# Optimization experiments

Hardware: AMD Instinct MI355X
Metric: run time of the kernel (lower is better)

## Reference

```python
import jax, jax.numpy as jnp
import numpy as np

B, S, D, H, AD, E = 4, 2048, 1024, 2048, 128, 8

def _ln(x, g, b, eps=1e-5):
    m = jnp.mean(x, axis=-1, keepdims=True)
    v = jnp.var(x, axis=-1, keepdims=True)
    return (x - m) * jax.lax.rsqrt(v + eps) * g + b

def setup_inputs() -> dict:
    key = jax.random.key(0)
    ks = jax.random.split(key, 12)
    scale = 1.0 / D ** 0.5
    ascale = scale * 0.01
    ead = 0.01 / AD ** 0.5
    return {
        'x': jax.random.normal(ks[0], (B, S, D), jnp.float32),
        'expert_weights': jax.random.uniform(ks[1], (B, S, E), jnp.float32),
        'Wu': jax.random.normal(ks[2], (H, D), jnp.float32) * scale,
        'bu': jnp.zeros((H,), jnp.float32),
        'Wg': jax.random.normal(ks[3], (H, D), jnp.float32) * scale,
        'bg': jnp.zeros((H,), jnp.float32),
        'Wd': jax.random.normal(ks[4], (D, H), jnp.float32) * scale,
        'bd': jnp.zeros((D,), jnp.float32),
        'Wpre': jax.random.normal(ks[5], (AD, D), jnp.float32) * ascale,
        'bpre': jnp.zeros((AD,), jnp.float32),
        'Wpost': jax.random.normal(ks[6], (AD, H), jnp.float32) * ascale,
        'bpost': jnp.zeros((AD,), jnp.float32),
        'ln_g': jnp.ones((AD,), jnp.float32),
        'ln_b': jnp.zeros((AD,), jnp.float32),
        'Wap': jax.random.normal(ks[7], (H, AD), jnp.float32) * ascale,
        'A': jax.random.normal(ks[8], (E, AD, AD), jnp.float32) * ead,
        'eg': jnp.ones((E, AD), jnp.float32),
        'eb': jnp.zeros((E, AD), jnp.float32),
        'Wp': jax.random.normal(ks[9], (H, AD), jnp.float32) * ead,
        'Wo': jax.random.normal(ks[10], (D, H), jnp.float32) * ead,
    }

def reference(x, expert_weights, Wu, bu, Wg, bg, Wd, bd, Wpre, bpre, Wpost, bpost, ln_g, ln_b, Wap, A, eg, eb, Wp, Wo):
    # ---- SharedExpertMLP ----
    up = x @ Wu.T + bu                      # [B,S,H]
    gate = x @ Wg.T + bg
    hidden = jax.nn.silu(gate) * up
    adapt_in = _ln(x @ Wpre.T + bpre, ln_g, ln_b)        # [B,S,AD]
    adapt_out = _ln(hidden @ Wpost.T + bpost, ln_g, ln_b)
    aw = jnp.einsum('bsa,bta->bst', adapt_in, adapt_out)  # [B,S,S]
    aw = jax.nn.silu(jnp.clip(aw, -5.0, 5.0))
    adapt = jnp.einsum('bst,bta->bsa', aw, adapt_in)
    hidden = hidden + 0.1 * (adapt @ Wap.T)
    shared = hidden @ Wd.T + bd                           # [B,S,D]
    # ---- expert branch (vectorized over experts) ----
    pre = x @ Wpre.T + bpre                               # [B,S,AD] (no adapt_norm here, as in torch)
    h = jnp.einsum('bsa,eca->ebsc', pre, A)               # per-expert adapter linear
    h = _ln(h, eg[:, None, None, :], eb[:, None, None, :])
    wmask = jnp.where(expert_weights > 0, expert_weights, 0.0)  # [B,S,E]
    hw = jnp.einsum('ebsa,bse->bsa', h, wmask)            # weighted combine before shared projections
    Wc = Wo @ Wp                                          # [D,AD]: output_proj(expert_proj(.))
    contrib = hw @ Wc.T                                   # [B,S,D]
    # sum_i w_i * (shared + 0.1*mask_i*expert_i) = shared*sum(w) + 0.1*sum(w_i*expert_i)
    return shared * jnp.sum(expert_weights, axis=-1, keepdims=True) + 0.1 * contrib
```

## Files before the change

kernel.cpp:

```cpp
#include <hip/hip_runtime.h>
#include <math.h>

#define BB 4
#define SS 2048
#define DD 1024
#define HH 2048
#define AD 128
#define EE 8
#define MM (BB*SS)
#define PS 136

typedef unsigned short u16;
typedef short bf16x8 __attribute__((ext_vector_type(8)));
typedef float f32x4 __attribute__((ext_vector_type(4)));
typedef float f32x16 __attribute__((ext_vector_type(16)));

__device__ __forceinline__ float silu_f(float x){ return x / (1.f + __expf(-x)); }

__device__ __forceinline__ u16 f2bf(float f){
    union { float f; unsigned u; } c; c.f = f;
    unsigned r = (c.u + 0x7FFFu + ((c.u >> 16) & 1u)) >> 16;
    return (u16)r;
}

__device__ __forceinline__ void gld16(const u16* g, u16* l){
    __builtin_amdgcn_global_load_lds((const __attribute__((address_space(1))) void*)g,
                                     (__attribute__((address_space(3))) void*)l, 16, 0, 0);
}

#define VMCNT(n) asm volatile("s_waitcnt vmcnt(" #n ")" ::: "memory")

__global__ __launch_bounds__(256,2) void mfma_sk(
    const u16* __restrict__ A, const u16* __restrict__ B, float* __restrict__ P,
    int M, int K, int S, long sA, long sB, long sC, long sSplit)
{
    __shared__ __align__(16) u16 As[128*32];
    __shared__ __align__(16) u16 Bs[128*32];
    const int t = threadIdx.x;
    const int lane = t & 63;
    const int wv = t >> 6;
    const int s = blockIdx.x;
    const int m0 = blockIdx.y * 128;
    const u16* Ab = A + (long)blockIdx.z * sA;
    const u16* Bb = B + (long)blockIdx.z * sB;
    const int srow = t >> 2, scol = (t & 3) * 8;
    const int Ks = K / S, kBeg = s * Ks;
    const u16* ga0 = Ab + (long)(m0 + srow) * K + scol + kBeg;
    const u16* ga1 = ga0 + 64L * K;
    const u16* gb0 = Bb + (long)srow * K + scol + kBeg;
    const u16* gb1 = gb0 + 64L * K;
    u16* la0 = As + t * 8;  u16* la1 = As + 2048 + t * 8;
    u16* lb0 = Bs + t * 8;  u16* lb1 = Bs + 2048 + t * 8;
    const int fr = lane & 15, q = lane >> 4;
    const int wm = (wv & 1) * 64, wn = (wv >> 1) * 64;

    f32x4 acc[4][4] = {};
    for (int k0 = 0; k0 < Ks; k0 += 32) {
        gld16(ga0 + k0, la0);
        gld16(ga1 + k0, la1);
        gld16(gb0 + k0, lb0);
        gld16(gb1 + k0, lb1);
        __syncthreads();
        bf16x8 af[4], bfr[4];
        #pragma unroll
        for (int i = 0; i < 4; ++i) af[i]  = *(const bf16x8*)&As[(wm + i*16 + fr)*32 + q*8];
        #pragma unroll
        for (int i = 0; i < 4; ++i) bfr[i] = *(const bf16x8*)&Bs[(wn + i*16 + fr)*32 + q*8];
        #pragma unroll
        for (int mi = 0; mi < 4; ++mi)
            #pragma unroll
            for (int ni = 0; ni < 4; ++ni)
                acc[mi][ni] = __builtin_amdgcn_mfma_f32_16x16x32_bf16(af[mi], bfr[ni], acc[mi][ni], 0, 0, 0);
        __syncthreads();
    }

    float* Pf = P + (long)s * sSplit + (long)blockIdx.z * sC;
    #pragma unroll
    for (int mi = 0; mi < 4; ++mi)
        #pragma unroll
        for (int ni = 0; ni < 4; ++ni) {
            const int col = wn + ni*16 + fr;
            #pragma unroll
            for (int r = 0; r < 4; ++r) {
                const int row = m0 + wm + mi*16 + q*4 + r;
                Pf[(long)row * 128 + col] = acc[mi][ni][r];
            }
        }
}

__global__ __launch_bounds__(512,2) void mfma_upgate(
    const u16* __restrict__ X, const u16* __restrict__ Wu_, const u16* __restrict__ Wg_,
    const float* __restrict__ bu, const float* __restrict__ bg, u16* __restrict__ H)
{
    __shared__ __align__(16) u16 lds[65536];
    const int t = threadIdx.x, lane = t & 63, wv = t >> 6;
    const int l31 = lane & 31, kh = lane >> 5;
    const int wr = wv >> 2, wc = wv & 3;
    const int m0 = blockIdx.y * 256, n0 = blockIdx.x * 128;

    const int srow = t >> 2;
    const int gcol = (((t & 3) ^ ((t >> 3) & 3)) * 8);
    const u16* gx0 = X   + (long)(m0 + srow) * DD + gcol;
    const u16* gx1 = gx0 + 128L * DD;
    const u16* gu  = Wu_ + (long)(n0 + srow) * DD + gcol;
    const u16* gg  = Wg_ + (long)(n0 + srow) * DD + gcol;
    const int st8 = t * 8;

    const int sw3 = (l31 >> 1) & 3;
    int offA[4][2], offB[2];
    #pragma unroll
    for (int m = 0; m < 4; ++m)
        #pragma unroll
        for (int ks = 0; ks < 2; ++ks)
            offA[m][ks] = (wr*128 + m*32 + l31)*32 + (((ks*2 + kh) ^ sw3) * 8);
    #pragma unroll
    for (int ks = 0; ks < 2; ++ks)
        offB[ks] = (wc*32 + l31)*32 + (((ks*2 + kh) ^ sw3) * 8);

    f32x16 accU[4] = {};
    f32x16 accG[4] = {};

    auto stage = [&](int tb) {
        u16* Lb = lds + (tb & 3) * 16384;
        const int k0 = tb * 32;
        gld16(gx0 + k0, Lb + st8);
        gld16(gx1 + k0, Lb + 4096 + st8);
        gld16(gu  + k0, Lb + 8192 + st8);
        gld16(gg  + k0, Lb + 12288 + st8);
    };

    auto compute = [&](int tb) {
        const u16* Lb = lds + (tb & 3) * 16384;
        bf16x8 a[4][2], uf[2], gf[2];
        #pragma unroll
        for (int ks = 0; ks < 2; ++ks) {
            uf[ks] = *(const bf16x8*)&Lb[8192  + offB[ks]];
            gf[ks] = *(const bf16x8*)&Lb[12288 + offB[ks]];
        }
        #pragma unroll
        for (int m = 0; m < 4; ++m)
            #pragma unroll
            for (int ks = 0; ks < 2; ++ks)
                a[m][ks] = *(const bf16x8*)&Lb[offA[m][ks]];
        __builtin_amdgcn_s_setprio(1);
        #pragma unroll
        for (int m = 0; m < 4; ++m)
            #pragma unroll
            for (int ks = 0; ks < 2; ++ks) {
                accU[m] = __builtin_amdgcn_mfma_f32_32x32x16_bf16(a[m][ks], uf[ks], accU[m], 0, 0, 0);
                accG[m] = __builtin_amdgcn_mfma_f32_32x32x16_bf16(a[m][ks], gf[ks], accG[m], 0, 0, 0);
            }
        __builtin_amdgcn_s_setprio(0);
    };

    stage(0); stage(1); stage(2);

    #pragma unroll 1
    for (int tt = 0; tt < 29; ++tt) {
        VMCNT(8);
        __builtin_amdgcn_s_barrier();
        __builtin_amdgcn_sched_barrier(0);
        stage(tt + 3);
        compute(tt);
    }
    VMCNT(8);
    __builtin_amdgcn_s_barrier();
    __builtin_amdgcn_sched_barrier(0);
    compute(29);
    VMCNT(4);
    __builtin_amdgcn_s_barrier();
    __builtin_amdgcn_sched_barrier(0);
    compute(30);
    VMCNT(0);
    __builtin_amdgcn_s_barrier();
    __builtin_amdgcn_sched_barrier(0);
    compute(31);

    const int col = n0 + wc*32 + l31;
    const float bub = bu[col], bgb = bg[col];
    u16* Hp = H + (long)(m0 + wr*128) * HH + col;
    #pragma unroll
    for (int m = 0; m < 4; ++m)
        #pragma unroll
        for (int r = 0; r < 16; ++r) {
            const int rowl = m*32 + (r & 3) + 8*(r >> 2) + 4*kh;
            const float u = accU[m][r] + bub;
            const float g = accG[m][r] + bgb;
            Hp[(long)rowl * HH] = f2bf(silu_f(g) * u);
        }
}

__global__ __launch_bounds__(256,2) void mfma_final(
    const u16* __restrict__ Hh, const u16* __restrict__ Wd_,
    const u16* __restrict__ Ac, const u16* __restrict__ Wcat,
    const float* __restrict__ bd, const float* __restrict__ sumw,
    float* __restrict__ out)
{
    __shared__ __align__(16) u16 lds[24576];
    const int t = threadIdx.x, lane = t & 63, wv = t >> 6;
    const int l31 = lane & 31, kh = lane >> 5;
    const int wr = wv & 1, wc = wv >> 1;
    const int m0 = blockIdx.y * 128, n0 = blockIdx.x * 128;

    const int srow = t >> 2;
    const int gcol = (((t & 3) ^ ((t >> 3) & 3)) * 8);
    const u16* gA1 = Hh   + (long)(m0 + srow) * HH  + gcol;
    const u16* gB1 = Wd_  + (long)(n0 + srow) * HH  + gcol;
    const u16* gA2 = Ac   + (long)(m0 + srow) * 256 + gcol;
    const u16* gB2 = Wcat + (long)(n0 + srow) * 256 + gcol;
    const int st8 = t * 8;

    const int sw3 = (l31 >> 1) & 3;
    int offA[2][2], offB[2][2];
    #pragma unroll
    for (int m = 0; m < 2; ++m)
        #pragma unroll
        for (int ks = 0; ks < 2; ++ks) {
            const int ko = ((ks*2 + kh) ^ sw3) * 8;
            offA[m][ks] =        (wr*64 + m*32 + l31)*32 + ko;
            offB[m][ks] = 4096 + (wc*64 + m*32 + l31)*32 + ko;
        }

    f32x16 acc[2][2]  = {};
    f32x16 acc2[2][2] = {};

    auto stage = [&](int tk) {
        u16* Lb = lds + (tk % 3) * 8192;
        if (tk < 64) {
            const int k0 = tk * 32;
            gld16(gA1 + k0,           Lb + st8);
            gld16(gA1 + 64L*HH + k0,  Lb + 2048 + st8);
            gld16(gB1 + k0,           Lb + 4096 + st8);
            gld16(gB1 + 64L*HH + k0,  Lb + 6144 + st8);
        } else {
            const int k0 = (tk - 64) * 32;
            gld16(gA2 + k0,           Lb + st8);
            gld16(gA2 + 64L*256 + k0, Lb + 2048 + st8);
            gld16(gB2 + k0,           Lb + 4096 + st8);
            gld16(gB2 + 64L*256 + k0, Lb + 6144 + st8);
        }
    };

    auto compute = [&](int tk, f32x16 (&A)[2][2]) {
        const u16* Lb = lds + (tk % 3) * 8192;
        bf16x8 a[2][2], b[2][2];
        #pragma unroll
        for (int m = 0; m < 2; ++m)
            #pragma unroll
            for (int ks = 0; ks < 2; ++ks) {
                a[m][ks] = *(const bf16x8*)&Lb[offA[m][ks]];
                b[m][ks] = *(const bf16x8*)&Lb[offB[m][ks]];
            }
        __builtin_amdgcn_s_setprio(1);
        #pragma unroll
        for (int m = 0; m < 2; ++m)
            #pragma unroll
            for (int n = 0; n < 2; ++n)
                #pragma unroll
                for (int ks = 0; ks < 2; ++ks)
                    A[m][n] = __builtin_amdgcn_mfma_f32_32x32x16_bf16(a[m][ks], b[n][ks], A[m][n], 0, 0, 0);
        __builtin_amdgcn_s_setprio(0);
    };

    stage(0); stage(1);
    #pragma unroll 1
    for (int tt = 0; tt < 70; ++tt) {
        VMCNT(4);
        __builtin_amdgcn_s_barrier();
        __builtin_amdgcn_sched_barrier(0);
        stage(tt + 2);
        if (tt < 64) compute(tt, acc); else compute(tt, acc2);
    }
    VMCNT(4);
    __builtin_amdgcn_s_barrier();
    __builtin_amdgcn_sched_barrier(0);
    compute(70, acc2);
    VMCNT(0);
    __builtin_amdgcn_s_barrier();
    __builtin_amdgcn_sched_barrier(0);
    compute(71, acc2);

    #pragma unroll
    for (int n = 0; n < 2; ++n) {
        const int col = n0 + wc*64 + n*32 + l31;
        const float bdc = bd[col];
        #pragma unroll
        for (int m = 0; m < 2; ++m)
            #pragma unroll
            for (int r = 0; r < 16; ++r) {
                const int row = m0 + wr*64 + m*32 + (r & 3) + 8*(r >> 2) + 4*kh;
                out[(long)row * DD + col] =
                    sumw[row] * (acc[m][n][r] + bdc) + 0.1f * acc2[m][n][r];
            }
    }
}

__global__ __launch_bounds__(256,2) void flash_pv(
    const u16* __restrict__ ai, const u16* __restrict__ ao,
    const u16* __restrict__ aiT, float* __restrict__ adaptP)
{
    __shared__ __align__(16) u16 As[128*32];
    __shared__ __align__(16) u16 Bs[128*32];
    __shared__ __align__(16) u16 Psh[128*PS];
    const int t = threadIdx.x, lane = t & 63, wv = t >> 6;
    const int fr = lane & 15, q = lane >> 4;
    const int wm = (wv & 1) * 64, wn = (wv >> 1) * 64;
    const int tg = blockIdx.x, s0 = blockIdx.y * 128, b = blockIdx.z;
    const u16* aib  = ai  + (long)b * SS * AD;
    const u16* aob  = ao  + (long)b * SS * AD;
    const u16* aiTb = aiT + (long)b * AD * SS;
    const int srow = t >> 2, scol = (t & 3) * 8;
    u16* la0 = As + t * 8;  u16* la1 = As + 2048 + t * 8;
    u16* lb0 = Bs + t * 8;  u16* lb1 = Bs + 2048 + t * 8;
    const u16* ga0 = aib + (long)(s0 + srow) * AD + scol;
    const u16* ga1 = ga0 + 64L * AD;

    f32x4 vacc[4][4] = {};
    for (int ti = 0; ti < 2; ++ti) {
        const int t0 = tg * 256 + ti * 128;
        const u16* gb0 = aob + (long)(t0 + srow) * AD + scol;
        const u16* gb1 = gb0 + 64L * AD;
        f32x4 acc[4][4] = {};
        for (int k0 = 0; k0 < AD; k0 += 32) {
            gld16(ga0 + k0, la0);
            gld16(ga1 + k0, la1);
            gld16(gb0 + k0, lb0);
            gld16(gb1 + k0, lb1);
            __syncthreads();
            bf16x8 af[4], bfr[4];
            #pragma unroll
            for (int i = 0; i < 4; ++i) af[i]  = *(const bf16x8*)&As[(wm + i*16 + fr)*32 + q*8];
            #pragma unroll
            for (int i = 0; i < 4; ++i) bfr[i] = *(const bf16x8*)&Bs[(wn + i*16 + fr)*32 + q*8];
            #pragma unroll
            for (int mi = 0; mi < 4; ++mi)
                #pragma unroll
                for (int ni = 0; ni < 4; ++ni)
                    acc[mi][ni] = __builtin_amdgcn_mfma_f32_16x16x32_bf16(af[mi], bfr[ni], acc[mi][ni], 0, 0, 0);
            __syncthreads();
        }
        #pragma unroll
        for (int mi = 0; mi < 4; ++mi)
            #pragma unroll
            for (int ni = 0; ni < 4; ++ni)
                #pragma unroll
                for (int r = 0; r < 4; ++r) {
                    float v = acc[mi][ni][r];
                    v = fminf(fmaxf(v, -5.f), 5.f);
                    Psh[(wm + mi*16 + q*4 + r)*PS + wn + ni*16 + fr] = f2bf(silu_f(v));
                }
        __syncthreads();
        #pragma unroll
        for (int kk = 0; kk < 4; ++kk) {
            bf16x8 pf[4], bi[4];
            #pragma unroll
            for (int mi = 0; mi < 4; ++mi)
                pf[mi] = *(const bf16x8*)&Psh[(wm + mi*16 + fr)*PS + kk*32 + q*8];
            #pragma unroll
            for (int ni = 0; ni < 4; ++ni)
                bi[ni] = *(const bf16x8*)&aiTb[(long)(wn + ni*16 + fr)*SS + t0 + kk*32 + q*8];
            #pragma unroll
            for (int mi = 0; mi < 4; ++mi)
                #pragma unroll
                for (int ni = 0; ni < 4; ++ni)
                    vacc[mi][ni] = __builtin_amdgcn_mfma_f32_16x16x32_bf16(pf[mi], bi[ni], vacc[mi][ni], 0, 0, 0);
        }
    }
    float* Pf = adaptP + (long)tg * MM * AD + (long)(b * SS + s0) * AD;
    #pragma unroll
    for (int mi = 0; mi < 4; ++mi)
        #pragma unroll
        for (int ni = 0; ni < 4; ++ni) {
            const int col = wn + ni*16 + fr;
            #pragma unroll
            for (int r = 0; r < 4; ++r) {
                const int row = wm + mi*16 + q*4 + r;
                Pf[(long)row * AD + col] = vacc[mi][ni][r];
            }
        }
}

__global__ __launch_bounds__(256) void scale_adapt(
    const float* __restrict__ P, const float* __restrict__ sumw, u16* __restrict__ acat)
{
    const int i = blockIdx.x * 256 + threadIdx.x;
    float4 v = ((const float4*)P)[i];
    #pragma unroll
    for (int tg = 1; tg < 8; ++tg) {
        const float4 w = ((const float4*)P)[i + (long)tg * (MM*AD/4)];
        v.x += w.x; v.y += w.y; v.z += w.z; v.w += w.w;
    }
    const long grow = i >> 5;
    const float sw = sumw[grow];
    ushort4 o;
    o.x = f2bf(sw*v.x); o.y = f2bf(sw*v.y); o.z = f2bf(sw*v.z); o.w = f2bf(sw*v.w);
    ((ushort4*)acat)[grow*64 + 32 + (i & 31)] = o;
}

__global__ __launch_bounds__(256) void expert_fused(
    const u16* __restrict__ pre, const u16* __restrict__ aexp,
    const float* __restrict__ ew, const float* __restrict__ eg,
    const float* __restrict__ eb, u16* __restrict__ acat,
    float* __restrict__ sumw)
{
    __shared__ float ewsh[32*8];
    __shared__ float egsh[8*128], ebsh[8*128];
    __shared__ float part[32*132];
    const int t = threadIdx.x, lane = t & 63, wv = t >> 6;
    const int fr = lane & 15, q = lane >> 4;
    const int wm = (wv & 1) * 16;
    const int e0 = (wv >> 1) * 4;
    const int m0 = blockIdx.x * 32;
    if (t < 64) {
        const int row = t >> 1, j = (t & 1)*4;
        *(float4*)&ewsh[row*8+j] = *(const float4*)&ew[(long)(m0+row)*EE + j];
    }
    {   const int e = t >> 5, c = (t & 31)*4;
        *(float4*)&egsh[e*128+c] = *(const float4*)&eg[e*128+c];
        *(float4*)&ebsh[e*128+c] = *(const float4*)&eb[e*128+c]; }
    __syncthreads();

    f32x4 hwacc[8] = {};
    for (int ee = 0; ee < 4; ++ee) {
        const int e = e0 + ee;
        f32x4 acc[8] = {};
        const u16* Ae = aexp + (long)e * AD * AD;
        #pragma unroll
        for (int ks = 0; ks < 4; ++ks) {
            bf16x8 af, bfr[8];
            af = *(const bf16x8*)&pre[(long)(m0 + wm + fr)*AD + ks*32 + q*8];
            #pragma unroll
            for (int ni = 0; ni < 8; ++ni)
                bfr[ni] = *(const bf16x8*)&Ae[(long)(ni*16 + fr)*AD + ks*32 + q*8];
            #pragma unroll
            for (int ni = 0; ni < 8; ++ni)
                acc[ni] = __builtin_amdgcn_mfma_f32_16x16x32_bf16(af, bfr[ni], acc[ni], 0, 0, 0);
        }
        #pragma unroll
        for (int r = 0; r < 4; ++r) {
            float s = 0.f, s2 = 0.f;
            #pragma unroll
            for (int ni = 0; ni < 8; ++ni) { const float v = acc[ni][r]; s += v; s2 += v*v; }
            #pragma unroll
            for (int msk = 1; msk < 16; msk <<= 1) {
                s  += __shfl_xor(s,  msk, 64);
                s2 += __shfl_xor(s2, msk, 64);
            }
            const float mean = s * (1.f/128.f);
            const float var  = s2 * (1.f/128.f) - mean*mean;
            const float rs   = rsqrtf(var + 1e-5f);
            const int rowl = wm + q*4 + r;
            float w = ewsh[rowl*8 + e]; w = w > 0.f ? w : 0.f;
            #pragma unroll
            for (int ni = 0; ni < 8; ++ni) {
                const int col = ni*16 + fr;
                hwacc[ni][r] += w * ((acc[ni][r] - mean) * rs * egsh[e*128+col] + ebsh[e*128+col]);
            }
        }
    }
    if (wv >= 2) {
        #pragma unroll
        for (int r = 0; r < 4; ++r) {
            const int rowl = wm + q*4 + r;
            #pragma unroll
            for (int ni = 0; ni < 8; ++ni)
                part[rowl*132 + ni*16 + fr] = hwacc[ni][r];
        }
    }
    __syncthreads();
    if (wv < 2) {
        #pragma unroll
        for (int r = 0; r < 4; ++r) {
            const int rowl = wm + q*4 + r;
            #pragma unroll
            for (int ni = 0; ni < 8; ++ni) {
                const float v = hwacc[ni][r] + part[rowl*132 + ni*16 + fr];
                acat[(long)(m0+rowl)*256 + ni*16 + fr] = f2bf(v);
            }
            if (fr == 0) {
                float sw = 0.f;
                #pragma unroll
                for (int j = 0; j < 8; ++j) sw += ewsh[rowl*8 + j];
                sumw[m0 + rowl] = sw;
            }
        }
    }
}

template<int S>
__global__ __launch_bounds__(128) void ln_reduce(
    const float* __restrict__ P, long sSplit, const float* __restrict__ bias,
    u16* __restrict__ raw, u16* __restrict__ ln_out,
    const float* __restrict__ g, const float* __restrict__ b)
{
    const int r = blockIdx.x, tid = threadIdx.x;
    float v = bias[tid];
    #pragma unroll
    for (int s = 0; s < S; ++s) v += P[(long)s * sSplit + (long)r * AD + tid];
    if (raw) raw[(long)r * AD + tid] = f2bf(v);
    __shared__ float red[AD], red2[AD];
    red[tid] = v; red2[tid] = v*v;
    __syncthreads();
    for (int s = 64; s > 0; s >>= 1) {
        if (tid < s) { red[tid] += red[tid+s]; red2[tid] += red2[tid+s]; }
        __syncthreads();
    }
    const float mean = red[0] * (1.f/AD);
    const float var  = red2[0] * (1.f/AD) - mean*mean;
    const float rs   = rsqrtf(var + 1e-5f);
    ln_out[(long)r * AD + tid] = f2bf((v - mean) * rs * g[tid] + b[tid]);
}

__global__ __launch_bounds__(256) void reduce_cat(
    const float* __restrict__ P, u16* __restrict__ Wcat)
{
    const int i = blockIdx.x * 256 + threadIdx.x;
    const int a4 = i & 31, z = (i >> 5) & 1, d = i >> 6;
    const float* src = P + (long)z * (16L*DD*AD) + (long)d * AD + a4*4;
    float4 v = *(const float4*)src;
    #pragma unroll
    for (int s = 1; s < 16; ++s) {
        const float4 w = *(const float4*)(src + (long)s * DD * AD);
        v.x += w.x; v.y += w.y; v.z += w.z; v.w += w.w;
    }
    ushort4 o; o.x=f2bf(v.x); o.y=f2bf(v.y); o.z=f2bf(v.z); o.w=f2bf(v.w);
    ((ushort4*)Wcat)[(long)d*64 + z*32 + a4] = o;
}

__global__ __launch_bounds__(256) void transpose6(
    const u16* __restrict__ wRaw, u16* __restrict__ wT,
    const u16* __restrict__ ai, u16* __restrict__ aiT)
{
    __shared__ u16 tile[32][33];
    const int z = blockIdx.z;
    const u16* in; u16* out;
    if (z < 2) { in = wRaw + (long)z * HH * AD; out = wT + (long)z * AD * HH; }
    else       { in = ai + (long)(z-2) * SS * AD; out = aiT + (long)(z-2) * AD * SS; }
    const int x0 = blockIdx.x * 32, y0 = blockIdx.y * 32;
    const int tx = threadIdx.x & 31, ty = threadIdx.x >> 5;
    #pragma unroll
    for (int j = 0; j < 4; ++j)
        tile[ty + j*8][tx] = in[(long)(y0 + ty + j*8) * AD + x0 + tx];
    __syncthreads();
    #pragma unroll
    for (int j = 0; j < 4; ++j)
        out[(long)(x0 + ty + j*8) * SS + y0 + tx] = tile[tx][ty + j*8];
}

struct Cvt5 { const float* in[5]; u16* out[5]; long cum[6]; };
__global__ __launch_bounds__(256) void cvt_pack(Cvt5 a)
{
    const long i = (long)blockIdx.x * 256 + threadIdx.x;
    if (i >= a.cum[5]) return;
    int s = 0;
    while (i >= a.cum[s+1]) ++s;
    const long j = i - a.cum[s];
    const float4 v = ((const float4*)a.in[s])[j];
    ushort4 o;
    o.x = f2bf(v.x); o.y = f2bf(v.y); o.z = f2bf(v.z); o.w = f2bf(v.w);
    ((ushort4*)a.out[s])[j] = o;
}

extern "C" void kernel_launch(void* const* d_in, const int* in_sizes, int n_in,
                              void* d_out, int out_size, void* d_ws, size_t ws_size,
                              hipStream_t stream) {
    const float* x    = (const float*)d_in[0];
    const float* ew   = (const float*)d_in[1];
    const float* Wu   = (const float*)d_in[2];
    const float* bu   = (const float*)d_in[3];
    const float* Wg   = (const float*)d_in[4];
    const float* bg   = (const float*)d_in[5];
    const float* Wd   = (const float*)d_in[6];
    const float* bd   = (const float*)d_in[7];
    const float* Wpre = (const float*)d_in[8];
    const float* bpre = (const float*)d_in[9];
    const float* Wpost= (const float*)d_in[10];
    const float* bpost= (const float*)d_in[11];
    const float* ln_g = (const float*)d_in[12];
    const float* ln_b = (const float*)d_in[13];
    const float* Wap  = (const float*)d_in[14];
    const float* Aex  = (const float*)d_in[15];
    const float* eg   = (const float*)d_in[16];
    const float* eb   = (const float*)d_in[17];
    const float* Wp   = (const float*)d_in[18];
    const float* Wo   = (const float*)d_in[19];
    float* out = (float*)d_out;

    char* p = (char*)d_ws;
    auto take = [&](long bytes) -> char* {
        char* r = p; p += (bytes + 255) & ~255L; return r;
    };
    u16* x_slot  = (u16*)take(16777216);
    u16* wslot   = (u16*)take((long)2*DD*HH*2);
    u16* wpre    = (u16*)take((long)AD*DD*2);
    u16* aex     = (u16*)take((long)EE*AD*AD*2);
    u16* pre_bf  = (u16*)take((long)MM*AD*2);
    u16* ai_bf   = (u16*)take((long)MM*AD*2);
    char* shareA = take(33554432);
    u16* acat    = (u16*)take((long)MM*256*2);
    float* sumw  = (float*)take((long)MM*4);
    u16* hidden  = (u16*)take((long)MM*HH*2);

    u16* x_bf    = x_slot;
    u16* aiT     = x_slot;
    u16* wRaw    = aiT  + 1048576;
    u16* wT      = wRaw + 524288;
    u16* wpost_w = wT   + 524288;
    u16* wcat    = wpost_w + 262144;
    u16* ao_bf   = wcat + 262144;
    float* preP   = (float*)shareA;
    float* wcP    = (float*)(shareA + 16777216);
    float* wpostP = (float*)shareA;
    float* adaptP = (float*)shareA;

    {
        Cvt5 a;
        a.in[0]=x;    a.out[0]=x_bf;              long n0=(long)MM*DD/4;
        a.in[1]=Wu;   a.out[1]=wslot;             long n1=(long)HH*DD/4;
        a.in[2]=Wg;   a.out[2]=wslot+(long)DD*HH; long n2=(long)HH*DD/4;
        a.in[3]=Wpre; a.out[3]=wpre;              long n3=(long)AD*DD/4;
        a.in[4]=Aex;  a.out[4]=aex;               long n4=(long)EE*AD*AD/4;
        a.cum[0]=0; a.cum[1]=n0; a.cum[2]=n0+n1; a.cum[3]=n0+n1+n2;
        a.cum[4]=n0+n1+n2+n3; a.cum[5]=n0+n1+n2+n3+n4;
        cvt_pack<<<dim3((a.cum[5]+255)/256), 256, 0, stream>>>(a);
    }
    mfma_sk<<<dim3(4, MM/128, 1), 256, 0, stream>>>(
        x_bf, wpre, preP, MM, DD, 4, 0, 0, 0, (long)MM*AD);
    ln_reduce<4><<<dim3(MM), 128, 0, stream>>>(preP, (long)MM*AD, bpre, pre_bf, ai_bf, ln_g, ln_b);
    expert_fused<<<dim3(MM/32), 256, 0, stream>>>(pre_bf, aex, ew, eg, eb, acat, sumw);
    mfma_upgate<<<dim3(HH/128, MM/256), 512, 0, stream>>>(
        x_bf, wslot, wslot+(long)DD*HH, bu, bg, hidden);
    {
        Cvt5 a;
        a.in[0]=Wo;    a.out[0]=wslot;             long n0=(long)DD*HH/4;
        a.in[1]=Wd;    a.out[1]=wslot+(long)DD*HH; long n1=(long)DD*HH/4;
        a.in[2]=Wpost; a.out[2]=wpost_w;           long n2=(long)AD*HH/4;
        a.in[3]=Wp;    a.out[3]=wRaw;              long n3=(long)HH*AD/4;
        a.in[4]=Wap;   a.out[4]=wRaw+(long)HH*AD;  long n4=(long)HH*AD/4;
        a.cum[0]=0; a.cum[1]=n0; a.cum[2]=n0+n1; a.cum[3]=n0+n1+n2;
        a.cum[4]=n0+n1+n2+n3; a.cum[5]=n0+n1+n2+n3+n4;
        cvt_pack<<<dim3((a.cum[5]+255)/256), 256, 0, stream>>>(a);
    }
    transpose6<<<dim3(4,64,6), 256, 0, stream>>>(wRaw, wT, ai_bf, aiT);
    mfma_sk<<<dim3(16, DD/128, 2), 256, 0, stream>>>(
        wslot, wT, wcP, DD, HH, 16, (long)DD*HH, (long)AD*HH, 16L*DD*AD, (long)DD*AD);
    reduce_cat<<<dim3(256), 256, 0, stream>>>(wcP, wcat);
    mfma_sk<<<dim3(8, MM/128, 1), 256, 0, stream>>>(
        hidden, wpost_w, wpostP, MM, HH, 8, 0, 0, 0, (long)MM*AD);
    ln_reduce<8><<<dim3(MM), 128, 0, stream>>>(wpostP, (long)MM*AD, bpost, nullptr, ao_bf, ln_g, ln_b);
    flash_pv<<<dim3(8, SS/128, BB), 256, 0, stream>>>(ai_bf, ao_bf, aiT, adaptP);
    scale_adapt<<<dim3((long)MM*AD/4/256), 256, 0, stream>>>(adaptP, sumw, acat);
    mfma_final<<<dim3(DD/128, MM/128), 256, 0, stream>>>(
        hidden, wslot+(long)DD*HH, acat, wcat, bd, sumw, out);
}
```

Before: 399.3 us.

## Pipeline split-K GEMM with 4-stage LDS buffering and swizzle; warp-shuffle LayerNorm reduce

Rewrites the split-K MFMA kernel to use a 4-deep LDS ring buffer with async global-to-LDS loads, vmcnt-based waits and an XOR swizzle on the K column to avoid bank conflicts. Previously every K step loaded into a single buffer and then waited at a barrier. The LayerNorm reduce now handles two rows per 256-thread block and uses wave shuffles instead of a shared-memory tree with many barriers. The hidden@Wpost split count drops from 8 to 4, which halves partial-sum traffic but leaves fewer blocks. LDS use grows to 64KB per block, which may limit occupancy.

```diff
diff --git a/kernel.cpp b/kernel.cpp
--- a/kernel.cpp
+++ b/kernel.cpp
@@ -34,8 +34,7 @@
     const u16* __restrict__ A, const u16* __restrict__ B, float* __restrict__ P,
     int M, int K, int S, long sA, long sB, long sC, long sSplit)
 {
-    __shared__ __align__(16) u16 As[128*32];
-    __shared__ __align__(16) u16 Bs[128*32];
+    __shared__ __align__(16) u16 lds[32768];
     const int t = threadIdx.x;
     const int lane = t & 63;
     const int wv = t >> 6;
@@ -43,36 +42,68 @@
     const int m0 = blockIdx.y * 128;
     const u16* Ab = A + (long)blockIdx.z * sA;
     const u16* Bb = B + (long)blockIdx.z * sB;
-    const int srow = t >> 2, scol = (t & 3) * 8;
+    const int srow = t >> 2;
+    const int gcol = (((t & 3) ^ ((t >> 3) & 3)) * 8);
     const int Ks = K / S, kBeg = s * Ks;
-    const u16* ga0 = Ab + (long)(m0 + srow) * K + scol + kBeg;
+    const int NT = Ks >> 5;
+    const u16* ga0 = Ab + (long)(m0 + srow) * K + gcol + kBeg;
     const u16* ga1 = ga0 + 64L * K;
-    const u16* gb0 = Bb + (long)srow * K + scol + kBeg;
+    const u16* gb0 = Bb + (long)srow * K + gcol + kBeg;
     const u16* gb1 = gb0 + 64L * K;
-    u16* la0 = As + t * 8;  u16* la1 = As + 2048 + t * 8;
-    u16* lb0 = Bs + t * 8;  u16* lb1 = Bs + 2048 + t * 8;
     const int fr = lane & 15, q = lane >> 4;
     const int wm = (wv & 1) * 64, wn = (wv >> 1) * 64;
+    const int st8 = t * 8;
+
+    const int sw3 = (fr >> 1) & 3;
+    const int koff = (q ^ sw3) * 8;
 
     f32x4 acc[4][4] = {};
-    for (int k0 = 0; k0 < Ks; k0 += 32) {
-        gld16(ga0 + k0, la0);
-        gld16(ga1 + k0, la1);
-        gld16(gb0 + k0, lb0);
-        gld16(gb1 + k0, lb1);
-        __syncthreads();
+
+    auto stage = [&](int tk) {
+        u16* Lb = lds + (tk & 3) * 8192;
+        const int k0 = tk * 32;
+        gld16(ga0 + k0, Lb + st8);
+        gld16(ga1 + k0, Lb + 2048 + st8);
+        gld16(gb0 + k0, Lb + 4096 + st8);
+        gld16(gb1 + k0, Lb + 6144 + st8);
+    };
+    auto compute = [&](int tk) {
+        const u16* Lb = lds + (tk & 3) * 8192;
         bf16x8 af[4], bfr[4];
         #pragma unroll
-        for (int i = 0; i < 4; ++i) af[i]  = *(const bf16x8*)&As[(wm + i*16 + fr)*32 + q*8];
-        #pragma unroll
-        for (int i = 0; i < 4; ++i) bfr[i] = *(const bf16x8*)&Bs[(wn + i*16 + fr)*32 + q*8];
+        for (int i = 0; i < 4; ++i) af[i]  = *(const bf16x8*)&Lb[(wm + i*16 + fr)*32 + koff];
+        #pragma unroll
+        for (int i = 0; i < 4; ++i) bfr[i] = *(const bf16x8*)&Lb[4096 + (wn + i*16 + fr)*32 + koff];
+        __builtin_amdgcn_s_setprio(1);
         #pragma unroll
         for (int mi = 0; mi < 4; ++mi)
             #pragma unroll
             for (int ni = 0; ni < 4; ++ni)
                 acc[mi][ni] = __builtin_amdgcn_mfma_f32_16x16x32_bf16(af[mi], bfr[ni], acc[mi][ni], 0, 0, 0);
-        __syncthreads();
-    }
+        __builtin_amdgcn_s_setprio(0);
+    };
+
+    stage(0); stage(1); stage(2);
+    #pragma unroll 1
+    for (int tt = 0; tt < NT - 3; ++tt) {
+        VMCNT(8);
+        __builtin_amdgcn_s_barrier();
+        __builtin_amdgcn_sched_barrier(0);
+        stage(tt + 3);
+        compute(tt);
+    }
+    VMCNT(8);
+    __builtin_amdgcn_s_barrier();
+    __builtin_amdgcn_sched_barrier(0);
+    compute(NT - 3);
+    VMCNT(4);
+    __builtin_amdgcn_s_barrier();
+    __builtin_amdgcn_sched_barrier(0);
+    compute(NT - 2);
+    VMCNT(0);
+    __builtin_amdgcn_s_barrier();
+    __builtin_amdgcn_sched_barrier(0);
+    compute(NT - 1);
 
     float* Pf = P + (long)s * sSplit + (long)blockIdx.z * sC;
     #pragma unroll
@@ -154,7 +185,6 @@
     };
 
     stage(0); stage(1); stage(2);
-
     #pragma unroll 1
     for (int tt = 0; tt < 29; ++tt) {
         VMCNT(8);
@@ -488,27 +518,34 @@
 }
 
 template<int S>
-__global__ __launch_bounds__(128) void ln_reduce(
+__global__ __launch_bounds__(256) void ln_reduce(
     const float* __restrict__ P, long sSplit, const float* __restrict__ bias,
     u16* __restrict__ raw, u16* __restrict__ ln_out,
     const float* __restrict__ g, const float* __restrict__ b)
 {
-    const int r = blockIdx.x, tid = threadIdx.x;
-    float v = bias[tid];
-    #pragma unroll
-    for (int s = 0; s < S; ++s) v += P[(long)s * sSplit + (long)r * AD + tid];
-    if (raw) raw[(long)r * AD + tid] = f2bf(v);
-    __shared__ float red[AD], red2[AD];
-    red[tid] = v; red2[tid] = v*v;
+    const int half = threadIdx.x >> 7;
+    const int c = threadIdx.x & 127;
+    const long r = (long)blockIdx.x * 2 + half;
+    float v = bias[c];
+    #pragma unroll
+    for (int s = 0; s < S; ++s) v += P[(long)s * sSplit + r * AD + c];
+    if (raw) raw[r * AD + c] = f2bf(v);
+    float s1 = v, s2 = v*v;
+    #pragma unroll
+    for (int m = 1; m < 64; m <<= 1) {
+        s1 += __shfl_xor(s1, m, 64);
+        s2 += __shfl_xor(s2, m, 64);
+    }
+    __shared__ float ws1[4], ws2[4];
+    const int wv = threadIdx.x >> 6;
+    if ((threadIdx.x & 63) == 0) { ws1[wv] = s1; ws2[wv] = s2; }
     __syncthreads();
-    for (int s = 64; s > 0; s >>= 1) {
-        if (tid < s) { red[tid] += red[tid+s]; red2[tid] += red2[tid+s]; }
-        __syncthreads();
-    }
-    const float mean = red[0] * (1.f/AD);
-    const float var  = red2[0] * (1.f/AD) - mean*mean;
+    const float S1 = ws1[half*2] + ws1[half*2+1];
+    const float S2 = ws2[half*2] + ws2[half*2+1];
+    const float mean = S1 * (1.f/AD);
+    const float var  = S2 * (1.f/AD) - mean*mean;
     const float rs   = rsqrtf(var + 1e-5f);
-    ln_out[(long)r * AD + tid] = f2bf((v - mean) * rs * g[tid] + b[tid]);
+    ln_out[r * AD + c] = f2bf((v - mean) * rs * g[c] + b[c]);
 }
 
 __global__ __launch_bounds__(256) void reduce_cat(
@@ -626,7 +663,7 @@
     }
     mfma_sk<<<dim3(4, MM/128, 1), 256, 0, stream>>>(
         x_bf, wpre, preP, MM, DD, 4, 0, 0, 0, (long)MM*AD);
-    ln_reduce<4><<<dim3(MM), 128, 0, stream>>>(preP, (long)MM*AD, bpre, pre_bf, ai_bf, ln_g, ln_b);
+    ln_reduce<4><<<dim3(MM/2), 256, 0, stream>>>(preP, (long)MM*AD, bpre, pre_bf, ai_bf, ln_g, ln_b);
     expert_fused<<<dim3(MM/32), 256, 0, stream>>>(pre_bf, aex, ew, eg, eb, acat, sumw);
     mfma_upgate<<<dim3(HH/128, MM/256), 512, 0, stream>>>(
         x_bf, wslot, wslot+(long)DD*HH, bu, bg, hidden);
@@ -645,9 +682,9 @@
     mfma_sk<<<dim3(16, DD/128, 2), 256, 0, stream>>>(
         wslot, wT, wcP, DD, HH, 16, (long)DD*HH, (long)AD*HH, 16L*DD*AD, (long)DD*AD);
     reduce_cat<<<dim3(256), 256, 0, stream>>>(wcP, wcat);
-    mfma_sk<<<dim3(8, MM/128, 1), 256, 0, stream>>>(
-        hidden, wpost_w, wpostP, MM, HH, 8, 0, 0, 0, (long)MM*AD);
-    ln_reduce<8><<<dim3(MM), 128, 0, stream>>>(wpostP, (long)MM*AD, bpost, nullptr, ao_bf, ln_g, ln_b);
+    mfma_sk<<<dim3(4, MM/128, 1), 256, 0, stream>>>(
+        hidden, wpost_w, wpostP, MM, HH, 4, 0, 0, 0, (long)MM*AD);
+    ln_reduce<4><<<dim3(MM/2), 256, 0, stream>>>(wpostP, (long)MM*AD, bpost, nullptr, ao_bf, ln_g, ln_b);
     flash_pv<<<dim3(8, SS/128, BB), 256, 0, stream>>>(ai_bf, ao_bf, aiT, adaptP);
     scale_adapt<<<dim3((long)MM*AD/4/256), 256, 0, stream>>>(adaptP, sumw, acat);
     mfma_final<<<dim3(DD/128, MM/128), 256, 0, stream>>>(
```

New measurement: 391.6 us. About the same (-1.9%).
